# Kernel optimization log

Hardware: AMD Instinct MI355X
Metric: run time of the kernel (lower is better)

Reference implementation:

```python
import jax, jax.numpy as jnp
import numpy as np

N = 1_000_000
F_IN = 3
GRID = 480
B = 2
EPS = 1e-5


def setup_inputs() -> dict:
    key = jax.random.key(0)
    ks = jax.random.split(key, 24)
    pt_fea = jax.random.normal(ks[0], (N, F_IN), dtype=jnp.float32)
    xy_ind = jax.random.randint(ks[1], (N, 2), 0, GRID, dtype=jnp.int64)

    # batch-id prepended (F.pad(xy_ind,(1,0),value=i_batch)), then unique rows.
    batch_id = np.arange(N, dtype=np.int64) // (N // B)
    ind_np = np.asarray(xy_ind)
    lin = batch_id * (GRID * GRID) + ind_np[:, 0] * GRID + ind_np[:, 1]
    unq_lin, unq_inv = np.unique(lin, return_inverse=True)  # sorted == lexsorted rows
    unq = np.stack([unq_lin // (GRID * GRID), (unq_lin // GRID) % GRID, unq_lin % GRID], axis=1)

    def lin_w(k, fin, fout):
        return 0.05 * jax.random.normal(k, (fin, fout), dtype=jnp.float32)

    dims = [F_IN, 64, 128, 256, 128]
    params = {}
    # BN affine params: bn0 on input, bn1..bn3 after linears 1..3
    for i, d in enumerate([F_IN, 64, 128, 256]):
        params[f"bn{i}_g"] = jnp.ones((d,), jnp.float32)
        params[f"bn{i}_b"] = jnp.zeros((d,), jnp.float32)
    for i in range(4):
        params[f"W{i+1}"] = lin_w(ks[2 + i], dims[i], dims[i + 1])
        params[f"b{i+1}"] = jnp.zeros((dims[i + 1],), jnp.float32)

    return dict(pt_fea=pt_fea, xy_ind=xy_ind,
                unq=jnp.asarray(unq, jnp.int64), unq_inv=jnp.asarray(unq_inv, jnp.int32),
                **params)


def _bn(x, g, b):
    # training-mode BatchNorm1d: batch stats, biased variance
    m = jnp.mean(x, axis=0)
    v = jnp.var(x, axis=0)
    return (x - m) * jax.lax.rsqrt(v + EPS) * g + b


def reference(pt_fea, xy_ind, unq, unq_inv,
              bn0_g, bn0_b, bn1_g, bn1_b, bn2_g, bn2_b, bn3_g, bn3_b,
              W1, b1, W2, b2, W3, b3, W4, b4):
    h = _bn(pt_fea, bn0_g, bn0_b)
    h = jax.nn.relu(_bn(h @ W1 + b1, bn1_g, bn1_b))
    h = jax.nn.relu(_bn(h @ W2 + b2, bn2_g, bn2_b))
    h = jax.nn.relu(_bn(h @ W3 + b3, bn3_g, bn3_b))
    h = h @ W4 + b4  # [N, 128]
    pooled = jax.ops.segment_max(h, unq_inv, num_segments=unq.shape[0])  # [U, 128]
    return unq, pooled
```

## Files before the change

kernel.cpp:

```cpp
#include <hip/hip_runtime.h>
#include <math.h>

typedef unsigned int u32;
typedef unsigned short u16;

#define EPS 1e-5f
#define PTS 64

#define S0 0
#define Q0 16
#define S1 32
#define Q1 96
#define S2 160
#define Q2 288
#define S3 416
#define Q3 672

#define Z4S 132

typedef __attribute__((ext_vector_type(8))) short v8s;
typedef __attribute__((ext_vector_type(4))) float v4f;
typedef __attribute__((ext_vector_type(2))) unsigned int v2u;

#define MFMA(a,b,c) __builtin_amdgcn_mfma_f32_16x16x32_bf16(a,b,c,0,0,0)

#define W2H 0
#define W2L 8192
#define W3H 16384
#define W3L 49152
#define W4H 81920
#define W4L 114688
__device__ __align__(16) u16 g_wfrag[147456];

__device__ float g_acc[1024];
__device__ float g_st[1024];
__device__ int   g_is64;
__device__ int   g_inv64;
__device__ int   g_umax;
__device__ long  g_U;

__device__ __forceinline__ float bf2f(u16 b){ return __uint_as_float(((u32)b) << 16); }
__device__ __forceinline__ u16 f2bf(float f){
  u32 u = __float_as_uint(f);
  return (u16)((u + 0x7fffu + ((u >> 16) & 1u)) >> 16);
}

__device__ __forceinline__ void atomicMaxF32(float* addr, float v){
  if (v == 0.f) v = 0.f;
  if (v >= 0.f) atomicMax((int*)addr, __float_as_int(v));
  else          atomicMin((u32*)addr, __float_as_uint(v));
}

__device__ __forceinline__ void waveRedArr(float* v, int n){
  #pragma unroll
  for (int off = 32; off > 0; off >>= 1)
    for (int i = 0; i < n; ++i) v[i] += __shfl_xor(v[i], off, 64);
}

template<int FIN, int FOUT>
__device__ __forceinline__ void chunk16(const u16* hsrc, int lane,
    const float* __restrict__ W, const float* __restrict__ bias,
    int j0, float acc[16])
{
  const int j0u = __builtin_amdgcn_readfirstlane(j0);
  #pragma unroll
  for (int jj = 0; jj < 16; ++jj) acc[jj] = bias[j0u + jj];
  #pragma unroll 4
  for (int k = 0; k < FIN; ++k){
    const float hk = bf2f(hsrc[k*PTS + lane]);
    const float* Wr = W + (long)k*FOUT + j0u;
    #pragma unroll
    for (int jj = 0; jj < 16; ++jj) acc[jj] = fmaf(hk, Wr[jj], acc[jj]);
  }
}

template<int FIN, int FOUT>
__device__ __forceinline__ void chunk16_acc(const u16* hsrc, int lane,
    const float* __restrict__ W, int j0, int k0, float acc[16])
{
  const int j0u = __builtin_amdgcn_readfirstlane(j0);
  #pragma unroll 4
  for (int k = 0; k < FIN; ++k){
    const float hk = bf2f(hsrc[k*PTS + lane]);
    const float* Wr = W + (long)(k0 + k)*FOUT + j0u;
    #pragma unroll
    for (int jj = 0; jj < 16; ++jj) acc[jj] = fmaf(hk, Wr[jj], acc[jj]);
  }
}

__device__ __forceinline__ void emitStats(float acc[16], bool valid, int lane, int j0,
                                          float* bs, float* bq){
  #pragma unroll
  for (int jj = 0; jj < 16; ++jj){
    float v = valid ? acc[jj] : 0.f;
    float sq[2] = {v, v*v};
    waveRedArr(sq, 2);
    if (lane == 0){ atomicAdd(&bs[j0+jj], sq[0]); atomicAdd(&bq[j0+jj], sq[1]); }
  }
}
__device__ __forceinline__ void emitH(float acc[16], int lane, int j0u, int soff, int qoff, u16* hdst){
  #pragma unroll
  for (int jj = 0; jj < 16; ++jj){
    float z = fmaxf(acc[jj]*g_st[soff+j0u+jj] + g_st[qoff+j0u+jj], 0.f);
    hdst[(j0u+jj)*PTS + lane] = f2bf(z);
  }
}

__global__ void kreset(){
  if (threadIdx.x == 0) g_umax = 0;
  for (int i = threadIdx.x; i < 1024; i += blockDim.x) g_acc[i] = 0.f;
}

__global__ void ksniff_inv(const u32* __restrict__ w, long nwords){
  __shared__ int any;
  if (threadIdx.x == 0) any = 0;
  __syncthreads();
  for (long i = 2L*threadIdx.x + 1; i < nwords; i += 2L*blockDim.x){
    if (w[i] != 0u){ any = 1; break; }
  }
  __syncthreads();
  if (threadIdx.x == 0) g_inv64 = (any == 0) ? 1 : 0;
}

__global__ __launch_bounds__(256) void ksegU(const void* __restrict__ invv, int N){
  const int inv64 = g_inv64;
  int m = 0;
  const int stride = gridDim.x*blockDim.x;
  if (inv64){
    const long long* q = (const long long*)invv;
    for (int i = blockIdx.x*blockDim.x + threadIdx.x; i < N; i += stride)
      m = max(m, (int)q[i]);
  } else {
    const int* q = (const int*)invv;
    for (int i = blockIdx.x*blockDim.x + threadIdx.x; i < N; i += stride)
      m = max(m, q[i]);
  }
  #pragma unroll
  for (int off = 32; off > 0; off >>= 1) m = max(m, __shfl_xor(m, off, 64));
  if ((threadIdx.x & 63) == 0) atomicMax(&g_umax, m);
}

__global__ void ksniff_unq(const u32* __restrict__ w){
  __shared__ int any;
  if (threadIdx.x == 0){ g_U = (long)g_umax + 1; any = 0; }
  __syncthreads();
  const long nwords = 3L*g_U;
  for (long i = 2L*threadIdx.x + 1; i < nwords; i += 2L*blockDim.x){
    if (w[i] != 0u){ any = 1; break; }
  }
  __syncthreads();
  if (threadIdx.x == 0) g_is64 = (any == 0) ? 1 : 0;
}

__global__ void kpoolinit(float* __restrict__ out, long outSize){
  const long U = g_U;
  const long lo = 3*U;
  const long hi = (131*U < outSize) ? 131*U : outSize;
  const long i0 = (long)blockIdx.x*blockDim.x + threadIdx.x;
  const long stride = (long)gridDim.x*blockDim.x;
  for (long i = lo + i0; i < hi; i += stride) out[i] = -INFINITY;
}

__global__ void kunq(float* __restrict__ out, const void* __restrict__ unqv, long outSize){
  const long U = g_U;
  const long n = (3*U < outSize) ? 3*U : outSize;
  const long i0 = (long)blockIdx.x*blockDim.x + threadIdx.x;
  const long stride = (long)gridDim.x*blockDim.x;
  if (g_is64){
    const long long* uq = (const long long*)unqv;
    for (long i = i0; i < n; i += stride) out[i] = (float)uq[i];
  } else {
    const int* uq = (const int*)unqv;
    for (long i = i0; i < n; i += stride) out[i] = (float)uq[i];
  }
}

__global__ __launch_bounds__(256) void kstats0(const float* __restrict__ x, int N){
  __shared__ float red[4][9];
  float a[9];
  #pragma unroll
  for (int i = 0; i < 9; ++i) a[i] = 0.f;
  const int stride = gridDim.x*blockDim.x;
  for (int p = blockIdx.x*blockDim.x + threadIdx.x; p < N; p += stride){
    float v0 = x[(size_t)p*3 + 0], v1 = x[(size_t)p*3 + 1], v2 = x[(size_t)p*3 + 2];
    a[0]+=v0; a[1]+=v1; a[2]+=v2;
    a[3]+=v0*v0; a[4]+=v1*v1; a[5]+=v2*v2;
    a[6]+=v0*v1; a[7]+=v0*v2; a[8]+=v1*v2;
  }
  waveRedArr(a, 9);
  const int w = threadIdx.x >> 6, lane = threadIdx.x & 63;
  if (lane == 0){
    #pragma unroll
    for (int i = 0; i < 9; ++i) red[w][i] = a[i];
  }
  __syncthreads();
  if (threadIdx.x < 9){
    float t = 0.f;
    #pragma unroll
    for (int k = 0; k < 4; ++k) t += red[k][threadIdx.x];
    const int c = threadIdx.x;
    atomicAdd(&g_acc[(c < 3) ? (S0 + c) : (Q0 + (c - 3))], t);
  }
}

__global__ void kfin(int dim, int soff, int qoff,
                     const float* __restrict__ g, const float* __restrict__ b, float invN){
  const int j = threadIdx.x;
  if (j >= dim) return;
  const float m = g_acc[soff+j]*invN;
  const float var = fmaxf(g_acc[qoff+j]*invN - m*m, 0.f);
  const float s = g[j]*rsqrtf(var + EPS);
  g_st[soff+j] = s;
  g_st[qoff+j] = b[j] - m*s;
}

__global__ void kfin1(const float* __restrict__ g1, const float* __restrict__ b1bn,
                      const float* __restrict__ W1, const float* __restrict__ b1lin,
                      float invN){
  const int j = threadIdx.x;
  if (j >= 64) return;
  float m0[3], s0[3], t0[3];
  #pragma unroll
  for (int c = 0; c < 3; ++c){
    m0[c] = g_acc[S0+c]*invN;
    s0[c] = g_st[S0+c];
    t0[c] = g_st[Q0+c];
  }
  float C[3][3];
  C[0][0] = g_acc[Q0+0]*invN - m0[0]*m0[0];
  C[1][1] = g_acc[Q0+1]*invN - m0[1]*m0[1];
  C[2][2] = g_acc[Q0+2]*invN - m0[2]*m0[2];
  C[0][1] = C[1][0] = g_acc[Q0+3]*invN - m0[0]*m0[1];
  C[0][2] = C[2][0] = g_acc[Q0+4]*invN - m0[0]*m0[2];
  C[1][2] = C[2][1] = g_acc[Q0+5]*invN - m0[1]*m0[2];

  float wj[3] = {W1[0*64 + j], W1[1*64 + j], W1[2*64 + j]};
  float mean = b1lin[j];
  #pragma unroll
  for (int c = 0; c < 3; ++c) mean += (m0[c]*s0[c] + t0[c])*wj[c];
  float var = 0.f;
  #pragma unroll
  for (int a = 0; a < 3; ++a)
    #pragma unroll
    for (int b = 0; b < 3; ++b)
      var += wj[a]*s0[a]*wj[b]*s0[b]*C[a][b];
  var = fmaxf(var, 0.f);
  const float sc = g1[j]*rsqrtf(var + EPS);
  g_st[S1+j] = sc;
  g_st[Q1+j] = b1bn[j] - mean*sc;
}


__global__ void kprep(const float* __restrict__ W2, const float* __restrict__ W3,
                      const float* __restrict__ W4){
  int t = blockIdx.x*blockDim.x + threadIdx.x;
  int frag = t >> 6, lane = t & 63;
  if (frag >= 144) return;
  const float* W; int F, fb, kb; u16 *hi, *lo;
  if (frag < 16){
    fb = frag >> 1; kb = frag & 1; W = W2; F = 128;
    size_t o = (size_t)((fb*2 + kb)*64 + lane)*8;
    hi = g_wfrag + W2H + o; lo = g_wfrag + W2L + o;
  } else if (frag < 80){
    int f = frag - 16; fb = f >> 2; kb = f & 3; W = W3; F = 256;
    size_t o = (size_t)((fb*4 + kb)*64 + lane)*8;
    hi = g_wfrag + W3H + o; lo = g_wfrag + W3L + o;
  } else {
    int f = frag - 80; fb = f >> 3; kb = f & 7; W = W4; F = 128;
    size_t o = (size_t)((fb*8 + kb)*64 + lane)*8;
    hi = g_wfrag + W4H + o; lo = g_wfrag + W4L + o;
  }
  const int feat = fb*16 + (lane & 15);
  const int k0 = kb*32 + (lane >> 4)*8;
  #pragma unroll
  for (int jj = 0; jj < 8; ++jj){
    float wv = W[(size_t)(k0 + jj)*F + feat];
    u16 h = f2bf(wv);
    hi[jj] = h;
    lo[jj] = f2bf(wv - bf2f(h));
  }
}

__global__ __launch_bounds__(256) void kpass2m(
    const float* __restrict__ x,
    const float* __restrict__ W1, const float* __restrict__ b1,
    const float* __restrict__ b2, u16* __restrict__ z2ws, int N)
{
  __shared__ __align__(16) u16 h1f[4096];
  __shared__ __align__(16) u16 z2f[8192];
  const int tid = threadIdx.x, w = tid >> 6, lane = tid & 63;
  const int g = lane >> 4, p15 = lane & 15;

  float s2[2][4], q2[2][4];
  #pragma unroll
  for (int f = 0; f < 2; ++f)
    #pragma unroll
    for (int r = 0; r < 4; ++r){ s2[f][r] = 0.f; q2[f][r] = 0.f; }

  const int j0u = __builtin_amdgcn_readfirstlane(w*16);
  const int nb = (N + 63) >> 6;
  for (int b = blockIdx.x; b < nb; b += gridDim.x){
    const int p = b*64 + lane;
    const bool valid = p < N;
    {
      float h0[3];
      #pragma unroll
      for (int c = 0; c < 3; ++c){
        float xv = valid ? x[(size_t)p*3 + c] : 0.f;
        h0[c] = xv*g_st[S0 + c] + g_st[Q0 + c];
      }
      float acc[16];
      #pragma unroll
      for (int jj = 0; jj < 16; ++jj) acc[jj] = b1[j0u + jj];
      #pragma unroll
      for (int k = 0; k < 3; ++k){
        const float* Wr = W1 + k*64 + j0u;
        #pragma unroll
        for (int jj = 0; jj < 16; ++jj) acc[jj] = fmaf(h0[k], Wr[jj], acc[jj]);
      }
      u16 hb[16];
      #pragma unroll
      for (int jj = 0; jj < 16; ++jj)
        hb[jj] = f2bf(fmaxf(acc[jj]*g_st[S1+j0u+jj] + g_st[Q1+j0u+jj], 0.f));
      const int kb = w >> 1;
      const int lA = ((2*w) & 3)*16 + p15;
      union { v8s v; u32 u[4]; } pa, pbk;
      #pragma unroll
      for (int q = 0; q < 4; ++q){
        pa.u[q]  = (u32)hb[2*q]     | ((u32)hb[2*q+1] << 16);
        pbk.u[q] = (u32)hb[8+2*q]   | ((u32)hb[8+2*q+1] << 16);
      }
      *(v8s*)(h1f + ((kb*4 + g)*64 + lA     )*8) = pa.v;
      *(v8s*)(h1f + ((kb*4 + g)*64 + lA + 16)*8) = pbk.v;
    }
    __syncthreads();
    #pragma unroll
    for (int f = 0; f < 2; ++f){
      const int fb = w*2 + f;
      const v4f bias = *(const v4f*)(b2 + fb*16 + g*4);
      v4f acc[4];
      #pragma unroll
      for (int pb = 0; pb < 4; ++pb) acc[pb] = bias;
      #pragma unroll
      for (int kb = 0; kb < 2; ++kb){
        const v8s Ah = *(const v8s*)(g_wfrag + W2H + (size_t)((fb*2+kb)*64 + lane)*8);
        const v8s Al = *(const v8s*)(g_wfrag + W2L + (size_t)((fb*2+kb)*64 + lane)*8);
        #pragma unroll
        for (int pb = 0; pb < 4; ++pb){
          const v8s B = *(const v8s*)(h1f + ((kb*4 + pb)*64 + lane)*8);
          acc[pb] = MFMA(Ah, B, acc[pb]);
          acc[pb] = MFMA(Al, B, acc[pb]);
        }
      }
      #pragma unroll
      for (int pb = 0; pb < 4; ++pb){
        const bool pv = (b*64 + pb*16 + p15) < N;
        u16 zb[4];
        #pragma unroll
        for (int r = 0; r < 4; ++r){
          float v = pv ? acc[pb][r] : 0.f;
          s2[f][r] += v; q2[f][r] += v*v;
          zb[r] = f2bf(acc[pb][r]);
        }
        const int kb2 = fb >> 1;
        const int lp = ((2*fb + (g >> 1)) & 3)*16 + p15;
        v2u dv; dv[0] = (u32)zb[0] | ((u32)zb[1] << 16);
        dv[1] = (u32)zb[2] | ((u32)zb[3] << 16);
        *(v2u*)(z2f + ((kb2*4 + pb)*64 + lp)*8 + 4*(g & 1)) = dv;
      }
    }
    __syncthreads();
    {
      u16* dst = z2ws + (size_t)b*8192;
      #pragma unroll
      for (int i = 0; i < 4; ++i){
        const int idx = (i*256 + tid)*8;
        *(v8s*)(dst + idx) = *(const v8s*)(z2f + idx);
      }
    }
    __syncthreads();
  }
  #pragma unroll
  for (int f = 0; f < 2; ++f)
    #pragma unroll
    for (int r = 0; r < 4; ++r){
      float s = s2[f][r], q = q2[f][r];
      #pragma unroll
      for (int off = 1; off < 16; off <<= 1){
        s += __shfl_xor(s, off, 64); q += __shfl_xor(q, off, 64);
      }
      if (p15 == 0){
        const int feat = (w*2 + f)*16 + g*4 + r;
        atomicAdd(&g_acc[S2 + feat], s);
        atomicAdd(&g_acc[Q2 + feat], q);
      }
    }
}

__global__ __launch_bounds__(256) void kpass3m(
    const u16* __restrict__ z2ws, const float* __restrict__ b3,
    u16* __restrict__ z3ws, int N)
{
  __shared__ __align__(16) u16 h2f[8192];
  __shared__ __align__(16) u16 z3f[16384];
  const int tid = threadIdx.x, w = tid >> 6, lane = tid & 63;
  const int g = lane >> 4, p15 = lane & 15;

  const int k0 = w*32 + g*8;
  const v4f sA = *(const v4f*)(g_st + S2 + k0);
  const v4f sB = *(const v4f*)(g_st + S2 + k0 + 4);
  const v4f tA = *(const v4f*)(g_st + Q2 + k0);
  const v4f tB = *(const v4f*)(g_st + Q2 + k0 + 4);

  float s3[4][4], q3[4][4];
  #pragma unroll
  for (int i = 0; i < 4; ++i)
    #pragma unroll
    for (int r = 0; r < 4; ++r){ s3[i][r] = 0.f; q3[i][r] = 0.f; }

  const int nb = (N + 63) >> 6;
  for (int b = blockIdx.x; b < nb; b += gridDim.x){
    #pragma unroll
    for (int pb = 0; pb < 4; ++pb){
      union { v8s v; u32 u[4]; } in, outv;
      in.v = *(const v8s*)(z2ws + (size_t)b*8192 + ((w*4 + pb)*64 + lane)*8);
      #pragma unroll
      for (int q = 0; q < 4; ++q){
        const int e = q*2;
        float z0 = bf2f((u16)(in.u[q] & 0xFFFFu));
        float z1 = bf2f((u16)(in.u[q] >> 16));
        const float sc0 = (e   < 4) ? sA[e]   : sB[e-4];
        const float sh0 = (e   < 4) ? tA[e]   : tB[e-4];
        const float sc1 = (e+1 < 4) ? sA[e+1] : sB[e-3];
        const float sh1 = (e+1 < 4) ? tA[e+1] : tB[e-3];
        z0 = fmaxf(fmaf(z0, sc0, sh0), 0.f);
        z1 = fmaxf(fmaf(z1, sc1, sh1), 0.f);
        outv.u[q] = (u32)f2bf(z0) | ((u32)f2bf(z1) << 16);
      }
      *(v8s*)(h2f + ((w*4 + pb)*64 + lane)*8) = outv.v;
    }
    __syncthreads();
    #pragma unroll
    for (int i = 0; i < 4; ++i){
      const int fb = w*4 + i;
      const v4f bias = *(const v4f*)(b3 + fb*16 + g*4);
      v4f acc[4];
      #pragma unroll
      for (int pb = 0; pb < 4; ++pb) acc[pb] = bias;
      #pragma unroll
      for (int kb = 0; kb < 4; ++kb){
        const v8s Ah = *(const v8s*)(g_wfrag + W3H + (size_t)((fb*4+kb)*64 + lane)*8);
        const v8s Al = *(const v8s*)(g_wfrag + W3L + (size_t)((fb*4+kb)*64 + lane)*8);
        #pragma unroll
        for (int pb = 0; pb < 4; ++pb){
          const v8s B = *(const v8s*)(h2f + ((kb*4 + pb)*64 + lane)*8);
          acc[pb] = MFMA(Ah, B, acc[pb]);
          acc[pb] = MFMA(Al, B, acc[pb]);
        }
      }
      #pragma unroll
      for (int pb = 0; pb < 4; ++pb){
        const bool pv = (b*64 + pb*16 + p15) < N;
        u16 zb[4];
        #pragma unroll
        for (int r = 0; r < 4; ++r){
          float v = pv ? acc[pb][r] : 0.f;
          s3[i][r] += v; q3[i][r] += v*v;
          zb[r] = f2bf(acc[pb][r]);
        }
        const int kb3 = fb >> 1;
        const int lp = ((2*fb + (g >> 1)) & 3)*16 + p15;
        v2u dv; dv[0] = (u32)zb[0] | ((u32)zb[1] << 16);
        dv[1] = (u32)zb[2] | ((u32)zb[3] << 16);
        *(v2u*)(z3f + ((kb3*4 + pb)*64 + lp)*8 + 4*(g & 1)) = dv;
      }
    }
    __syncthreads();
    {
      u16* dst = z3ws + (size_t)b*16384;
      #pragma unroll
      for (int i2 = 0; i2 < 8; ++i2){
        const int idx = (i2*256 + tid)*8;
        *(v8s*)(dst + idx) = *(const v8s*)(z3f + idx);
      }
    }
    __syncthreads();
  }
  #pragma unroll
  for (int i = 0; i < 4; ++i)
    #pragma unroll
    for (int r = 0; r < 4; ++r){
      float s = s3[i][r], q = q3[i][r];
      #pragma unroll
      for (int off = 1; off < 16; off <<= 1){
        s += __shfl_xor(s, off, 64); q += __shfl_xor(q, off, 64);
      }
      if (p15 == 0){
        const int feat = (w*4 + i)*16 + g*4 + r;
        atomicAdd(&g_acc[S3 + feat], s);
        atomicAdd(&g_acc[Q3 + feat], q);
      }
    }
}

__global__ __launch_bounds__(256) void kpass4m(
    const void* __restrict__ unq_inv_v, const float* __restrict__ b4,
    const u16* __restrict__ z3ws, float* __restrict__ out, int N, long outSize)
{
  __shared__ __align__(16) u16 buf[16896];
  __shared__ int seg_s[64];
  u16* const h3f = buf;
  float* const z4 = (float*)buf;

  const long U = g_U;
  const int inv64 = g_inv64;
  const long loEl = 3*U;
  const long hiEl = (131*U < outSize) ? 131*U : outSize;
  const int tid = threadIdx.x, w = tid >> 6, lane = tid & 63;
  const int g = lane >> 4, p15 = lane & 15;

  const int k0a = w*64 + g*8;
  const v4f sA0 = *(const v4f*)(g_st + S3 + k0a);
  const v4f sA1 = *(const v4f*)(g_st + S3 + k0a + 4);
  const v4f tA0 = *(const v4f*)(g_st + Q3 + k0a);
  const v4f tA1 = *(const v4f*)(g_st + Q3 + k0a + 4);
  const v4f sB0 = *(const v4f*)(g_st + S3 + k0a + 32);
  const v4f sB1 = *(const v4f*)(g_st + S3 + k0a + 36);
  const v4f tB0 = *(const v4f*)(g_st + Q3 + k0a + 32);
  const v4f tB1 = *(const v4f*)(g_st + Q3 + k0a + 36);

  const int nb = (N + 63) >> 6;
  for (int b = blockIdx.x; b < nb; b += gridDim.x){
    const int p = b*64 + lane;
    const bool valid = p < N;

    #pragma unroll
    for (int kk = 0; kk < 2; ++kk){
      const int kb3 = 2*w + kk;
      #pragma unroll
      for (int pb = 0; pb < 4; ++pb){
        union { v8s v; u32 u[4]; } in, outv;
        in.v = *(const v8s*)(z3ws + (size_t)b*16384 + ((kb3*4 + pb)*64 + lane)*8);
        #pragma unroll
        for (int q = 0; q < 4; ++q){
          const int e = q*2;
          float z0 = bf2f((u16)(in.u[q] & 0xFFFFu));
          float z1 = bf2f((u16)(in.u[q] >> 16));
          const float sc0 = kk ? ((e   < 4) ? sB0[e]   : sB1[e-4]) : ((e   < 4) ? sA0[e]   : sA1[e-4]);
          const float sh0 = kk ? ((e   < 4) ? tB0[e]   : tB1[e-4]) : ((e   < 4) ? tA0[e]   : tA1[e-4]);
          const float sc1 = kk ? ((e+1 < 4) ? sB0[e+1] : sB1[e-3]) : ((e+1 < 4) ? sA0[e+1] : sA1[e-3]);
          const float sh1 = kk ? ((e+1 < 4) ? tB0[e+1] : tB1[e-3]) : ((e+1 < 4) ? tA0[e+1] : tA1[e-3]);
          z0 = fmaxf(fmaf(z0, sc0, sh0), 0.f);
          z1 = fmaxf(fmaf(z1, sc1, sh1), 0.f);
          outv.u[q] = (u32)f2bf(z0) | ((u32)f2bf(z1) << 16);
        }
        *(v8s*)(h3f + ((kb3*4 + pb)*64 + lane)*8) = outv.v;
      }
    }
    if (w == 0){
      long seg = -1;
      if (valid){
        if (inv64) seg = (long)((const long long*)unq_inv_v)[p];
        else       seg = (long)((const int*)unq_inv_v)[p];
      }
      seg_s[lane] = (seg >= 0 && seg < U &&
                     loEl + seg*128 + 128 <= hiEl) ? (int)seg : -1;
    }
    __syncthreads();

    v4f acc[2][4];
    #pragma unroll
    for (int f = 0; f < 2; ++f){
      const int fb = w*2 + f;
      const v4f bias = *(const v4f*)(b4 + fb*16 + g*4);
      #pragma unroll
      for (int pb = 0; pb < 4; ++pb) acc[f][pb] = bias;
      #pragma unroll
      for (int kb = 0; kb < 8; ++kb){
        const v8s Ah = *(const v8s*)(g_wfrag + W4H + (size_t)((fb*8+kb)*64 + lane)*8);
        const v8s Al = *(const v8s*)(g_wfrag + W4L + (size_t)((fb*8+kb)*64 + lane)*8);
        #pragma unroll
        for (int pb = 0; pb < 4; ++pb){
          const v8s B = *(const v8s*)(h3f + ((kb*4 + pb)*64 + lane)*8);
          acc[f][pb] = MFMA(Ah, B, acc[f][pb]);
          acc[f][pb] = MFMA(Al, B, acc[f][pb]);
        }
      }
    }
    __syncthreads();
    #pragma unroll
    for (int f = 0; f < 2; ++f){
      const int fb = w*2 + f;
      #pragma unroll
      for (int pb = 0; pb < 4; ++pb)
        *(v4f*)(z4 + (pb*16 + p15)*Z4S + fb*16 + g*4) = acc[f][pb];
    }
    __syncthreads();
    #pragma unroll 4
    for (int pt2 = 0; pt2 < 64; pt2 += 2){
      const int pt = pt2 + (tid >> 7);
      const int fI = tid & 127;
      const int sg = seg_s[pt];
      if (sg >= 0)
        atomicMaxF32(out + loEl + (long)sg*128 + fI, z4[pt*Z4S + fI]);
    }
    __syncthreads();
  }
}

template<int WS2>
__global__ __launch_bounds__(256) void kpass2(
    const float* __restrict__ x,
    const float* __restrict__ W1, const float* __restrict__ b1,
    const float* __restrict__ W2, const float* __restrict__ b2,
    u16* __restrict__ z2ws, int N)
{
  __shared__ u16 h1s[64*PTS];
  __shared__ float bs[256], bq[256];
  const int tid = threadIdx.x, w = tid >> 6, lane = tid & 63;
  for (int i = tid; i < 256; i += 256){ bs[i] = 0.f; bq[i] = 0.f; }
  __syncthreads();
  const int nb = (N + PTS - 1) / PTS;
  for (int b = blockIdx.x; b < nb; b += gridDim.x){
    const int p = b*PTS + lane;
    const bool valid = p < N;
    {
      float h0[3];
      #pragma unroll
      for (int c = 0; c < 3; ++c){
        float xv = valid ? x[(size_t)p*3 + c] : 0.f;
        h0[c] = xv*g_st[S0 + c] + g_st[Q0 + c];
      }
      const int j0u = __builtin_amdgcn_readfirstlane(w*16);
      float acc[16];
      #pragma unroll
      for (int jj = 0; jj < 16; ++jj) acc[jj] = b1[j0u + jj];
      #pragma unroll
      for (int k = 0; k < 3; ++k){
        const float* Wr = W1 + k*64 + j0u;
        #pragma unroll
        for (int jj = 0; jj < 16; ++jj) acc[jj] = fmaf(h0[k], Wr[jj], acc[jj]);
      }
      emitH(acc, lane, j0u, S1, Q1, h1s);
    }
    __syncthreads();
    #pragma unroll
    for (int c = 0; c < 2; ++c){
      const int j0 = w*32 + c*16;
      float acc[16];
      chunk16<64,128>(h1s, lane, W2, b2, j0, acc);
      if constexpr (WS2){
        const int j0u = __builtin_amdgcn_readfirstlane(j0);
        u16* q = z2ws + (size_t)b*8192 + (size_t)j0u*64 + lane;
        #pragma unroll
        for (int jj = 0; jj < 16; ++jj) q[jj*64] = f2bf(acc[jj]);
      }
      emitStats(acc, valid, lane, j0, bs, bq);
    }
    __syncthreads();
  }
  for (int j = tid; j < 128; j += 256){
    atomicAdd(&g_acc[S2 + j], bs[j]);
    atomicAdd(&g_acc[Q2 + j], bq[j]);
  }
}

template<int MODE>
__global__ __launch_bounds__(256) void kpass3(
    const float* __restrict__ x,
    const float* __restrict__ W1, const float* __restrict__ b1,
    const float* __restrict__ W2, const float* __restrict__ b2,
    const float* __restrict__ W3, const float* __restrict__ b3,
    u16* __restrict__ z3ws, int N)
{
  __shared__ u16 buf[12288];
  __shared__ float bs[256], bq[256];
  u16* const h2s = buf;
  u16* const h1s = buf + 8192;
  const int tid = threadIdx.x, w = tid >> 6, lane = tid & 63;
  for (int i = tid; i < 256; i += 256){ bs[i] = 0.f; bq[i] = 0.f; }
  __syncthreads();
  const int nb = (N + PTS - 1) / PTS;
  for (int b = blockIdx.x; b < nb; b += gridDim.x){
    const int p = b*PTS + lane;
    const bool valid = p < N;
    {
      float h0[3];
      #pragma unroll
      for (int c = 0; c < 3; ++c){
        float xv = valid ? x[(size_t)p*3 + c] : 0.f;
        h0[c] = xv*g_st[S0 + c] + g_st[Q0 + c];
      }
      const int j0u = __builtin_amdgcn_readfirstlane(w*16);
      float acc[16];
      #pragma unroll
      for (int jj = 0; jj < 16; ++jj) acc[jj] = b1[j0u + jj];
      #pragma unroll
      for (int k = 0; k < 3; ++k){
        const float* Wr = W1 + k*64 + j0u;
        #pragma unroll
        for (int jj = 0; jj < 16; ++jj) acc[jj] = fmaf(h0[k], Wr[jj], acc[jj]);
      }
      emitH(acc, lane, j0u, S1, Q1, h1s);
    }
    __syncthreads();
    #pragma unroll
    for (int c = 0; c < 2; ++c){
      const int j0 = w*32 + c*16;
      float acc[16];
      chunk16<64,128>(h1s, lane, W2, b2, j0, acc);
      emitH(acc, lane, __builtin_amdgcn_readfirstlane(j0), S2, Q2, h2s);
    }
    __syncthreads();
    #pragma unroll
    for (int c = 0; c < 4; ++c){
      const int j0 = w*64 + c*16;
      float acc[16];
      chunk16<128,256>(h2s, lane, W3, b3, j0, acc);
      if constexpr (MODE == 1){
        const int j0u = __builtin_amdgcn_readfirstlane(j0);
        u16* q = z3ws + (size_t)b*16384 + (size_t)j0u*64 + lane;
        #pragma unroll
        for (int jj = 0; jj < 16; ++jj) q[jj*64] = f2bf(acc[jj]);
      }
      emitStats(acc, valid, lane, j0, bs, bq);
    }
    __syncthreads();
  }
  for (int j = tid; j < 256; j += 256){
    atomicAdd(&g_acc[S3 + j], bs[j]);
    atomicAdd(&g_acc[Q3 + j], bq[j]);
  }
}

template<int MODE>
__global__ __launch_bounds__(256) void kpass4(
    const float* __restrict__ x, const void* __restrict__ unq_inv_v,
    const float* __restrict__ W1, const float* __restrict__ b1,
    const float* __restrict__ W2, const float* __restrict__ b2,
    const float* __restrict__ W3, const float* __restrict__ b3,
    const float* __restrict__ W4, const float* __restrict__ b4,
    u16* __restrict__ z3ws, float* __restrict__ out, int N, long outSize)
{
  __shared__ u16 buf[16896];
  __shared__ int seg_s[64];
  u16* const h1s = buf + 8192;
  u16* const h2s = buf;
  u16* const h3h = buf + 8192;
  u16* const h3s = buf;
  float* const z4 = (float*)buf;
  const long U = g_U;
  const int inv64 = g_inv64;
  const long loEl = 3*U;
  const long hiEl = (131*U < outSize) ? 131*U : outSize;
  const int tid = threadIdx.x, w = tid >> 6, lane = tid & 63;
  const int nb = (N + PTS - 1) / PTS;
  for (int b = blockIdx.x; b < nb; b += gridDim.x){
    const int p = b*PTS + lane;
    const bool valid = p < N;
    float accA[16], accB[16];
    if constexpr (MODE == 0){
      {
        float h0[3];
        #pragma unroll
        for (int c = 0; c < 3; ++c){
          float xv = valid ? x[(size_t)p*3 + c] : 0.f;
          h0[c] = xv*g_st[S0 + c] + g_st[Q0 + c];
        }
        const int j0u = __builtin_amdgcn_readfirstlane(w*16);
        float acc[16];
        #pragma unroll
        for (int jj = 0; jj < 16; ++jj) acc[jj] = b1[j0u + jj];
        #pragma unroll
        for (int k = 0; k < 3; ++k){
          const float* Wr = W1 + k*64 + j0u;
          #pragma unroll
          for (int jj = 0; jj < 16; ++jj) acc[jj] = fmaf(h0[k], Wr[jj], acc[jj]);
        }
        emitH(acc, lane, j0u, S1, Q1, h1s);
      }
      __syncthreads();
      #pragma unroll
      for (int c = 0; c < 2; ++c){
        const int j0 = w*32 + c*16;
        float acc[16];
        chunk16<64,128>(h1s, lane, W2, b2, j0, acc);
        emitH(acc, lane, __builtin_amdgcn_readfirstlane(j0), S2, Q2, h2s);
      }
      const int jA = __builtin_amdgcn_readfirstlane(w*32);
      #pragma unroll
      for (int jj = 0; jj < 16; ++jj){ accA[jj] = b4[jA + jj]; accB[jj] = b4[jA + 16 + jj]; }
      #pragma unroll
      for (int half = 0; half < 2; ++half){
        __syncthreads();
        #pragma unroll
        for (int c = 0; c < 2; ++c){
          const int j0 = half*128 + w*32 + c*16;
          float acc[16];
          chunk16<128,256>(h2s, lane, W3, b3, j0, acc);
          const int j0u = __builtin_amdgcn_readfirstlane(j0);
          const int r0 = j0u - half*128;
          #pragma unroll
          for (int jj = 0; jj < 16; ++jj){
            float z = fmaxf(acc[jj]*g_st[S3+j0u+jj] + g_st[Q3+j0u+jj], 0.f);
            h3h[(r0+jj)*PTS + lane] = f2bf(z);
          }
        }
        __syncthreads();
        chunk16_acc<128,128>(h3h, lane, W4, w*32,      half*128, accA);
        chunk16_acc<128,128>(h3h, lane, W4, w*32 + 16, half*128, accB);
      }
    } else {
      const int j0u = __builtin_amdgcn_readfirstlane(w*64);
      const u16* q = z3ws + (size_t)b*16384 + (size_t)j0u*64 + lane;
      #pragma unroll 8
      for (int mm = 0; mm < 64; ++mm){
        const int m = j0u + mm;
        float z = bf2f(q[mm*64]);
        z = fmaxf(z*g_st[S3 + m] + g_st[Q3 + m], 0.f);
        h3s[m*PTS + lane] = f2bf(z);
      }
      __syncthreads();
      chunk16<256,128>(h3s, lane, W4, b4, w*32,      accA);
      chunk16<256,128>(h3s, lane, W4, b4, w*32 + 16, accB);
    }
    if (w == 0){
      long seg = -1;
      if (valid){
        if (inv64) seg = (long)((const long long*)unq_inv_v)[p];
        else       seg = (long)((const int*)unq_inv_v)[p];
      }
      seg_s[lane] = (seg >= 0 && seg < U &&
                     loEl + seg*128 + 128 <= hiEl) ? (int)seg : -1;
    }
    __syncthreads();
    {
      float4* dst = (float4*)&z4[lane*Z4S + w*32];
      dst[0] = make_float4(accA[ 0],accA[ 1],accA[ 2],accA[ 3]);
      dst[1] = make_float4(accA[ 4],accA[ 5],accA[ 6],accA[ 7]);
      dst[2] = make_float4(accA[ 8],accA[ 9],accA[10],accA[11]);
      dst[3] = make_float4(accA[12],accA[13],accA[14],accA[15]);
      dst[4] = make_float4(accB[ 0],accB[ 1],accB[ 2],accB[ 3]);
      dst[5] = make_float4(accB[ 4],accB[ 5],accB[ 6],accB[ 7]);
      dst[6] = make_float4(accB[ 8],accB[ 9],accB[10],accB[11]);
      dst[7] = make_float4(accB[12],accB[13],accB[14],accB[15]);
    }
    __syncthreads();
    #pragma unroll 4
    for (int pt2 = 0; pt2 < 64; pt2 += 2){
      const int pt = pt2 + (tid >> 7);
      const int f = tid & 127;
      const int sg = seg_s[pt];
      if (sg >= 0)
        atomicMaxF32(out + loEl + (long)sg*128 + f, z4[pt*Z4S + f]);
    }
    __syncthreads();
  }
}

extern "C" void kernel_launch(void* const* d_in, const int* in_sizes, int n_in,
                              void* d_out, int out_size, void* d_ws, size_t ws_size,
                              hipStream_t stream)
{
  const float* x       = (const float*)d_in[0];
  const void*  unq     = d_in[2];
  const void*  unq_inv = d_in[3];
  const float* bn_g[4] = {(const float*)d_in[4], (const float*)d_in[6], (const float*)d_in[8], (const float*)d_in[10]};
  const float* bn_b[4] = {(const float*)d_in[5], (const float*)d_in[7], (const float*)d_in[9], (const float*)d_in[11]};
  const float* W1 = (const float*)d_in[12]; const float* b1 = (const float*)d_in[13];
  const float* W2 = (const float*)d_in[14]; const float* b2 = (const float*)d_in[15];
  const float* W3 = (const float*)d_in[16]; const float* b3 = (const float*)d_in[17];
  const float* W4 = (const float*)d_in[18]; const float* b4 = (const float*)d_in[19];

  const int N = in_sizes[0] / 3;
  float* out = (float*)d_out;
  const float invN = 1.0f / (float)N;
  const long outSize = (long)out_size;

  const size_t nb64 = (size_t)((N + 63) / 64);
  u16* z3ws = (u16*)d_ws;
  u16* z2ws = z3ws + nb64*16384;
  const size_t need1 = nb64*16384*sizeof(u16);
  const size_t need2 = nb64*(16384+8192)*sizeof(u16);
  const int wsLevel = (ws_size >= need2) ? 2 : (ws_size >= need1) ? 1 : 0;

  kreset<<<1, 1024, 0, stream>>>();
  ksniff_inv<<<1, 1024, 0, stream>>>((const u32*)unq_inv, (long)N);
  ksegU<<<512, 256, 0, stream>>>(unq_inv, N);
  ksniff_unq<<<1, 1024, 0, stream>>>((const u32*)unq);
  kpoolinit<<<2048, 256, 0, stream>>>(out, outSize);

  kstats0<<<1024, 256, 0, stream>>>(x, N);
  kfin<<<1, 256, 0, stream>>>(3, S0, Q0, bn_g[0], bn_b[0], invN);
  kfin1<<<1, 64, 0, stream>>>(bn_g[1], bn_b[1], W1, b1, invN);

  if (wsLevel == 2){
    kprep<<<36, 256, 0, stream>>>(W2, W3, W4);
    kpass2m<<<2048, 256, 0, stream>>>(x, W1, b1, b2, z2ws, N);
    kfin<<<1, 256, 0, stream>>>(128, S2, Q2, bn_g[2], bn_b[2], invN);
    kpass3m<<<1536, 256, 0, stream>>>(z2ws, b3, z3ws, N);
    kfin<<<1, 256, 0, stream>>>(256, S3, Q3, bn_g[3], bn_b[3], invN);
    kpass4m<<<1024, 256, 0, stream>>>(unq_inv, b4, z3ws, out, N, outSize);
  } else if (wsLevel == 1){
    kpass2<0><<<2048, 256, 0, stream>>>(x, W1,b1,W2,b2, z2ws, N);
    kfin<<<1, 256, 0, stream>>>(128, S2, Q2, bn_g[2], bn_b[2], invN);
    kpass3<1><<<1536, 256, 0, stream>>>(x, W1,b1,W2,b2,W3,b3, z3ws, N);
    kfin<<<1, 256, 0, stream>>>(256, S3, Q3, bn_g[3], bn_b[3], invN);
    kpass4<2><<<1024, 256, 0, stream>>>(x, unq_inv, W1,b1,W2,b2,W3,b3,W4,b4, z3ws, out, N, outSize);
  } else {
    kpass2<0><<<2048, 256, 0, stream>>>(x, W1,b1,W2,b2, z2ws, N);
    kfin<<<1, 256, 0, stream>>>(128, S2, Q2, bn_g[2], bn_b[2], invN);
    kpass3<0><<<1536, 256, 0, stream>>>(x, W1,b1,W2,b2,W3,b3, z3ws, N);
    kfin<<<1, 256, 0, stream>>>(256, S3, Q3, bn_g[3], bn_b[3], invN);
    kpass4<0><<<1024, 256, 0, stream>>>(x, unq_inv, W1,b1,W2,b2,W3,b3,W4,b4, z3ws, out, N, outSize);
  }

  kunq<<<2048, 256, 0, stream>>>(out, unq, outSize);
}
```

Baseline: 1.554 ms.

## Counting-sort points by segment so pooling reduces runs locally before writing

Adds a histogram, prefix scan and scatter that build a permutation ordering points by segment id. The MLP passes then run on the permuted order, and the final pooling pass reduces each run of equal segments within a 64-point tile in registers. Interior runs get a plain store and only runs that cross a tile boundary use an atomic max, cutting the per-element atomic traffic. The cost is four extra kernels, including a single-block serial scan over all segments, plus gathered loads of x. The old fallback paths for smaller workspace are removed.

```diff
diff --git a/kernel.cpp b/kernel.cpp
--- a/kernel.cpp
+++ b/kernel.cpp
@@ -248,6 +248,66 @@
   const float sc = g1[j]*rsqrtf(var + EPS);
   g_st[S1+j] = sc;
   g_st[Q1+j] = b1bn[j] - mean*sc;
+}
+
+__global__ void kinitsort(u32* __restrict__ cnt, u32* __restrict__ perm,
+                          int* __restrict__ segSorted, long nPos){
+  const long U = g_U;
+  const long i0 = (long)blockIdx.x*blockDim.x + threadIdx.x;
+  const long stride = (long)gridDim.x*blockDim.x;
+  for (long i = i0; i < U; i += stride) cnt[i] = 0u;
+  for (long i = i0; i < nPos; i += stride){ perm[i] = 0u; segSorted[i] = -1; }
+}
+
+__global__ __launch_bounds__(256) void khist(const void* __restrict__ invv,
+                                             u32* __restrict__ cnt, int N){
+  const int inv64 = g_inv64;
+  const long U = g_U;
+  const int stride = gridDim.x*blockDim.x;
+  for (int i = blockIdx.x*blockDim.x + threadIdx.x; i < N; i += stride){
+    long s = inv64 ? (long)((const long long*)invv)[i] : (long)((const int*)invv)[i];
+    if (s >= 0 && s < U) atomicAdd(&cnt[s], 1u);
+  }
+}
+
+__global__ __launch_bounds__(1024) void kscan(u32* __restrict__ cnt){
+  __shared__ u32 sh[1024];
+  __shared__ u32 carry;
+  const long U = g_U;
+  if (threadIdx.x == 0) carry = 0u;
+  __syncthreads();
+  for (long base = 0; base < U; base += 1024){
+    const long i = base + threadIdx.x;
+    const u32 v = (i < U) ? cnt[i] : 0u;
+    sh[threadIdx.x] = v;
+    __syncthreads();
+    #pragma unroll
+    for (int off = 1; off < 1024; off <<= 1){
+      u32 t = (threadIdx.x >= off) ? sh[threadIdx.x - off] : 0u;
+      __syncthreads();
+      sh[threadIdx.x] += t;
+      __syncthreads();
+    }
+    if (i < U) cnt[i] = carry + (sh[threadIdx.x] - v);
+    __syncthreads();
+    if (threadIdx.x == 0) carry += sh[1023];
+    __syncthreads();
+  }
+}
+
+__global__ __launch_bounds__(256) void kscatter(const void* __restrict__ invv,
+    u32* __restrict__ cnt, u32* __restrict__ perm, int* __restrict__ segSorted, int N){
+  const int inv64 = g_inv64;
+  const long U = g_U;
+  const int stride = gridDim.x*blockDim.x;
+  for (int i = blockIdx.x*blockDim.x + threadIdx.x; i < N; i += stride){
+    long s = inv64 ? (long)((const long long*)invv)[i] : (long)((const int*)invv)[i];
+    if (s >= 0 && s < U){
+      u32 pos = atomicAdd(&cnt[s], 1u);
+      perm[pos] = (u32)i;
+      segSorted[pos] = (int)s;
+    }
+  }
 }
 
 
@@ -281,10 +341,12 @@
   }
 }
 
+template<int SORT>
 __global__ __launch_bounds__(256) void kpass2m(
     const float* __restrict__ x,
     const float* __restrict__ W1, const float* __restrict__ b1,
-    const float* __restrict__ b2, u16* __restrict__ z2ws, int N)
+    const float* __restrict__ b2, u16* __restrict__ z2ws,
+    const u32* __restrict__ perm, int N)
 {
   __shared__ __align__(16) u16 h1f[4096];
   __shared__ __align__(16) u16 z2f[8192];
@@ -303,10 +365,11 @@
     const int p = b*64 + lane;
     const bool valid = p < N;
     {
+      const long ps = SORT ? (long)perm[p] : (long)p;
       float h0[3];
       #pragma unroll
       for (int c = 0; c < 3; ++c){
-        float xv = valid ? x[(size_t)p*3 + c] : 0.f;
+        float xv = valid ? x[ps*3 + c] : 0.f;
         h0[c] = xv*g_st[S0 + c] + g_st[Q0 + c];
       }
       float acc[16];
@@ -503,12 +566,15 @@
     }
 }
 
+template<int SORT>
 __global__ __launch_bounds__(256) void kpass4m(
-    const void* __restrict__ unq_inv_v, const float* __restrict__ b4,
+    const void* __restrict__ unq_inv_v, const int* __restrict__ segSorted,
+    const float* __restrict__ b4,
     const u16* __restrict__ z3ws, float* __restrict__ out, int N, long outSize)
 {
   __shared__ __align__(16) u16 buf[16896];
   __shared__ int seg_s[64];
+  __shared__ int segPrev_s, segNext_s;
   u16* const h3f = buf;
   float* const z4 = (float*)buf;
 
@@ -530,6 +596,7 @@
   const v4f tB1 = *(const v4f*)(g_st + Q3 + k0a + 36);
 
   const int nb = (N + 63) >> 6;
+  const long nPos = (long)nb*64;
   for (int b = blockIdx.x; b < nb; b += gridDim.x){
     const int p = b*64 + lane;
     const bool valid = p < N;
@@ -558,13 +625,24 @@
       }
     }
     if (w == 0){
-      long seg = -1;
-      if (valid){
-        if (inv64) seg = (long)((const long long*)unq_inv_v)[p];
-        else       seg = (long)((const int*)unq_inv_v)[p];
-      }
-      seg_s[lane] = (seg >= 0 && seg < U &&
-                     loEl + seg*128 + 128 <= hiEl) ? (int)seg : -1;
+      int sg = -1;
+      if constexpr (SORT){
+        sg = segSorted[(long)b*64 + lane];
+      } else {
+        if (valid){
+          long s = inv64 ? (long)((const long long*)unq_inv_v)[p]
+                         : (long)((const int*)unq_inv_v)[p];
+          sg = (int)s;
+        }
+      }
+      seg_s[lane] = (sg >= 0 && sg < U &&
+                     loEl + (long)sg*128 + 128 <= hiEl) ? sg : -1;
+      if constexpr (SORT){
+        if (lane == 0){
+          segPrev_s = (b > 0) ? segSorted[(long)b*64 - 1] : -2;
+          segNext_s = ((long)b*64 + 64 < nPos) ? segSorted[(long)b*64 + 64] : -2;
+        }
+      }
     }
     __syncthreads();
 
@@ -596,263 +674,33 @@
         *(v4f*)(z4 + (pb*16 + p15)*Z4S + fb*16 + g*4) = acc[f][pb];
     }
     __syncthreads();
-    #pragma unroll 4
-    for (int pt2 = 0; pt2 < 64; pt2 += 2){
-      const int pt = pt2 + (tid >> 7);
-      const int fI = tid & 127;
-      const int sg = seg_s[pt];
-      if (sg >= 0)
-        atomicMaxF32(out + loEl + (long)sg*128 + fI, z4[pt*Z4S + fI]);
-    }
-    __syncthreads();
-  }
-}
-
-template<int WS2>
-__global__ __launch_bounds__(256) void kpass2(
-    const float* __restrict__ x,
-    const float* __restrict__ W1, const float* __restrict__ b1,
-    const float* __restrict__ W2, const float* __restrict__ b2,
-    u16* __restrict__ z2ws, int N)
-{
-  __shared__ u16 h1s[64*PTS];
-  __shared__ float bs[256], bq[256];
-  const int tid = threadIdx.x, w = tid >> 6, lane = tid & 63;
-  for (int i = tid; i < 256; i += 256){ bs[i] = 0.f; bq[i] = 0.f; }
-  __syncthreads();
-  const int nb = (N + PTS - 1) / PTS;
-  for (int b = blockIdx.x; b < nb; b += gridDim.x){
-    const int p = b*PTS + lane;
-    const bool valid = p < N;
-    {
-      float h0[3];
-      #pragma unroll
-      for (int c = 0; c < 3; ++c){
-        float xv = valid ? x[(size_t)p*3 + c] : 0.f;
-        h0[c] = xv*g_st[S0 + c] + g_st[Q0 + c];
-      }
-      const int j0u = __builtin_amdgcn_readfirstlane(w*16);
-      float acc[16];
-      #pragma unroll
-      for (int jj = 0; jj < 16; ++jj) acc[jj] = b1[j0u + jj];
-      #pragma unroll
-      for (int k = 0; k < 3; ++k){
-        const float* Wr = W1 + k*64 + j0u;
-        #pragma unroll
-        for (int jj = 0; jj < 16; ++jj) acc[jj] = fmaf(h0[k], Wr[jj], acc[jj]);
-      }
-      emitH(acc, lane, j0u, S1, Q1, h1s);
-    }
-    __syncthreads();
-    #pragma unroll
-    for (int c = 0; c < 2; ++c){
-      const int j0 = w*32 + c*16;
-      float acc[16];
-      chunk16<64,128>(h1s, lane, W2, b2, j0, acc);
-      if constexpr (WS2){
-        const int j0u = __builtin_amdgcn_readfirstlane(j0);
-        u16* q = z2ws + (size_t)b*8192 + (size_t)j0u*64 + lane;
-        #pragma unroll
-        for (int jj = 0; jj < 16; ++jj) q[jj*64] = f2bf(acc[jj]);
-      }
-      emitStats(acc, valid, lane, j0, bs, bq);
-    }
-    __syncthreads();
-  }
-  for (int j = tid; j < 128; j += 256){
-    atomicAdd(&g_acc[S2 + j], bs[j]);
-    atomicAdd(&g_acc[Q2 + j], bq[j]);
-  }
-}
-
-template<int MODE>
-__global__ __launch_bounds__(256) void kpass3(
-    const float* __restrict__ x,
-    const float* __restrict__ W1, const float* __restrict__ b1,
-    const float* __restrict__ W2, const float* __restrict__ b2,
-    const float* __restrict__ W3, const float* __restrict__ b3,
-    u16* __restrict__ z3ws, int N)
-{
-  __shared__ u16 buf[12288];
-  __shared__ float bs[256], bq[256];
-  u16* const h2s = buf;
-  u16* const h1s = buf + 8192;
-  const int tid = threadIdx.x, w = tid >> 6, lane = tid & 63;
-  for (int i = tid; i < 256; i += 256){ bs[i] = 0.f; bq[i] = 0.f; }
-  __syncthreads();
-  const int nb = (N + PTS - 1) / PTS;
-  for (int b = blockIdx.x; b < nb; b += gridDim.x){
-    const int p = b*PTS + lane;
-    const bool valid = p < N;
-    {
-      float h0[3];
-      #pragma unroll
-      for (int c = 0; c < 3; ++c){
-        float xv = valid ? x[(size_t)p*3 + c] : 0.f;
-        h0[c] = xv*g_st[S0 + c] + g_st[Q0 + c];
-      }
-      const int j0u = __builtin_amdgcn_readfirstlane(w*16);
-      float acc[16];
-      #pragma unroll
-      for (int jj = 0; jj < 16; ++jj) acc[jj] = b1[j0u + jj];
-      #pragma unroll
-      for (int k = 0; k < 3; ++k){
-        const float* Wr = W1 + k*64 + j0u;
-        #pragma unroll
-        for (int jj = 0; jj < 16; ++jj) acc[jj] = fmaf(h0[k], Wr[jj], acc[jj]);
-      }
-      emitH(acc, lane, j0u, S1, Q1, h1s);
-    }
-    __syncthreads();
-    #pragma unroll
-    for (int c = 0; c < 2; ++c){
-      const int j0 = w*32 + c*16;
-      float acc[16];
-      chunk16<64,128>(h1s, lane, W2, b2, j0, acc);
-      emitH(acc, lane, __builtin_amdgcn_readfirstlane(j0), S2, Q2, h2s);
-    }
-    __syncthreads();
-    #pragma unroll
-    for (int c = 0; c < 4; ++c){
-      const int j0 = w*64 + c*16;
-      float acc[16];
-      chunk16<128,256>(h2s, lane, W3, b3, j0, acc);
-      if constexpr (MODE == 1){
-        const int j0u = __builtin_amdgcn_readfirstlane(j0);
-        u16* q = z3ws + (size_t)b*16384 + (size_t)j0u*64 + lane;
-        #pragma unroll
-        for (int jj = 0; jj < 16; ++jj) q[jj*64] = f2bf(acc[jj]);
-      }
-      emitStats(acc, valid, lane, j0, bs, bq);
-    }
-    __syncthreads();
-  }
-  for (int j = tid; j < 256; j += 256){
-    atomicAdd(&g_acc[S3 + j], bs[j]);
-    atomicAdd(&g_acc[Q3 + j], bq[j]);
-  }
-}
-
-template<int MODE>
-__global__ __launch_bounds__(256) void kpass4(
-    const float* __restrict__ x, const void* __restrict__ unq_inv_v,
-    const float* __restrict__ W1, const float* __restrict__ b1,
-    const float* __restrict__ W2, const float* __restrict__ b2,
-    const float* __restrict__ W3, const float* __restrict__ b3,
-    const float* __restrict__ W4, const float* __restrict__ b4,
-    u16* __restrict__ z3ws, float* __restrict__ out, int N, long outSize)
-{
-  __shared__ u16 buf[16896];
-  __shared__ int seg_s[64];
-  u16* const h1s = buf + 8192;
-  u16* const h2s = buf;
-  u16* const h3h = buf + 8192;
-  u16* const h3s = buf;
-  float* const z4 = (float*)buf;
-  const long U = g_U;
-  const int inv64 = g_inv64;
-  const long loEl = 3*U;
-  const long hiEl = (131*U < outSize) ? 131*U : outSize;
-  const int tid = threadIdx.x, w = tid >> 6, lane = tid & 63;
-  const int nb = (N + PTS - 1) / PTS;
-  for (int b = blockIdx.x; b < nb; b += gridDim.x){
-    const int p = b*PTS + lane;
-    const bool valid = p < N;
-    float accA[16], accB[16];
-    if constexpr (MODE == 0){
-      {
-        float h0[3];
-        #pragma unroll
-        for (int c = 0; c < 3; ++c){
-          float xv = valid ? x[(size_t)p*3 + c] : 0.f;
-          h0[c] = xv*g_st[S0 + c] + g_st[Q0 + c];
-        }
-        const int j0u = __builtin_amdgcn_readfirstlane(w*16);
-        float acc[16];
-        #pragma unroll
-        for (int jj = 0; jj < 16; ++jj) acc[jj] = b1[j0u + jj];
-        #pragma unroll
-        for (int k = 0; k < 3; ++k){
-          const float* Wr = W1 + k*64 + j0u;
-          #pragma unroll
-          for (int jj = 0; jj < 16; ++jj) acc[jj] = fmaf(h0[k], Wr[jj], acc[jj]);
-        }
-        emitH(acc, lane, j0u, S1, Q1, h1s);
-      }
-      __syncthreads();
-      #pragma unroll
-      for (int c = 0; c < 2; ++c){
-        const int j0 = w*32 + c*16;
-        float acc[16];
-        chunk16<64,128>(h1s, lane, W2, b2, j0, acc);
-        emitH(acc, lane, __builtin_amdgcn_readfirstlane(j0), S2, Q2, h2s);
-      }
-      const int jA = __builtin_amdgcn_readfirstlane(w*32);
-      #pragma unroll
-      for (int jj = 0; jj < 16; ++jj){ accA[jj] = b4[jA + jj]; accB[jj] = b4[jA + 16 + jj]; }
-      #pragma unroll
-      for (int half = 0; half < 2; ++half){
-        __syncthreads();
-        #pragma unroll
-        for (int c = 0; c < 2; ++c){
-          const int j0 = half*128 + w*32 + c*16;
-          float acc[16];
-          chunk16<128,256>(h2s, lane, W3, b3, j0, acc);
-          const int j0u = __builtin_amdgcn_readfirstlane(j0);
-          const int r0 = j0u - half*128;
-          #pragma unroll
-          for (int jj = 0; jj < 16; ++jj){
-            float z = fmaxf(acc[jj]*g_st[S3+j0u+jj] + g_st[Q3+j0u+jj], 0.f);
-            h3h[(r0+jj)*PTS + lane] = f2bf(z);
-          }
-        }
-        __syncthreads();
-        chunk16_acc<128,128>(h3h, lane, W4, w*32,      half*128, accA);
-        chunk16_acc<128,128>(h3h, lane, W4, w*32 + 16, half*128, accB);
+
+    if constexpr (SORT){
+      const int sPrev = segPrev_s, sNext = segNext_s;
+      #pragma unroll 1
+      for (int pt2 = 0; pt2 < 64; pt2 += 2){
+        const int pt = pt2 + (tid >> 7);
+        const int fI = tid & 127;
+        const int sg = seg_s[pt];
+        if (sg >= 0 && (pt == 0 || seg_s[pt-1] != sg)){
+          float m = z4[pt*Z4S + fI];
+          int e = pt + 1;
+          while (e < 64 && seg_s[e] == sg){ m = fmaxf(m, z4[e*Z4S + fI]); ++e; }
+          const long row = loEl + (long)sg*128 + fI;
+          const bool bnd = (pt == 0 && sPrev == sg) || (e == 64 && sNext == sg);
+          if (bnd) atomicMaxF32(out + row, m);
+          else     out[row] = (m == 0.f) ? 0.f : m;
+        }
       }
     } else {
-      const int j0u = __builtin_amdgcn_readfirstlane(w*64);
-      const u16* q = z3ws + (size_t)b*16384 + (size_t)j0u*64 + lane;
-      #pragma unroll 8
-      for (int mm = 0; mm < 64; ++mm){
-        const int m = j0u + mm;
-        float z = bf2f(q[mm*64]);
-        z = fmaxf(z*g_st[S3 + m] + g_st[Q3 + m], 0.f);
-        h3s[m*PTS + lane] = f2bf(z);
-      }
-      __syncthreads();
-      chunk16<256,128>(h3s, lane, W4, b4, w*32,      accA);
-      chunk16<256,128>(h3s, lane, W4, b4, w*32 + 16, accB);
-    }
-    if (w == 0){
-      long seg = -1;
-      if (valid){
-        if (inv64) seg = (long)((const long long*)unq_inv_v)[p];
-        else       seg = (long)((const int*)unq_inv_v)[p];
-      }
-      seg_s[lane] = (seg >= 0 && seg < U &&
-                     loEl + seg*128 + 128 <= hiEl) ? (int)seg : -1;
-    }
-    __syncthreads();
-    {
-      float4* dst = (float4*)&z4[lane*Z4S + w*32];
-      dst[0] = make_float4(accA[ 0],accA[ 1],accA[ 2],accA[ 3]);
-      dst[1] = make_float4(accA[ 4],accA[ 5],accA[ 6],accA[ 7]);
-      dst[2] = make_float4(accA[ 8],accA[ 9],accA[10],accA[11]);
-      dst[3] = make_float4(accA[12],accA[13],accA[14],accA[15]);
-      dst[4] = make_float4(accB[ 0],accB[ 1],accB[ 2],accB[ 3]);
-      dst[5] = make_float4(accB[ 4],accB[ 5],accB[ 6],accB[ 7]);
-      dst[6] = make_float4(accB[ 8],accB[ 9],accB[10],accB[11]);
-      dst[7] = make_float4(accB[12],accB[13],accB[14],accB[15]);
-    }
-    __syncthreads();
-    #pragma unroll 4
-    for (int pt2 = 0; pt2 < 64; pt2 += 2){
-      const int pt = pt2 + (tid >> 7);
-      const int f = tid & 127;
-      const int sg = seg_s[pt];
-      if (sg >= 0)
-        atomicMaxF32(out + loEl + (long)sg*128 + f, z4[pt*Z4S + f]);
+      #pragma unroll 4
+      for (int pt2 = 0; pt2 < 64; pt2 += 2){
+        const int pt = pt2 + (tid >> 7);
+        const int fI = tid & 127;
+        const int sg = seg_s[pt];
+        if (sg >= 0)
+          atomicMaxF32(out + loEl + (long)sg*128 + fI, z4[pt*Z4S + fI]);
+      }
     }
     __syncthreads();
   }
@@ -878,11 +726,15 @@
   const long outSize = (long)out_size;
 
   const size_t nb64 = (size_t)((N + 63) / 64);
+  const size_t nPos = nb64 * 64;
   u16* z3ws = (u16*)d_ws;
   u16* z2ws = z3ws + nb64*16384;
-  const size_t need1 = nb64*16384*sizeof(u16);
+  u32* permW = (u32*)(z2ws + nb64*8192);
+  int* segSortedW = (int*)(permW + nPos);
+  u32* cntW = (u32*)(segSortedW + nPos);
   const size_t need2 = nb64*(16384+8192)*sizeof(u16);
-  const int wsLevel = (ws_size >= need2) ? 2 : (ws_size >= need1) ? 1 : 0;
+  const size_t need3 = need2 + (nPos*2 + (size_t)N)*4;
+  const int wsLevel = (ws_size >= need3) ? 3 : (ws_size >= need2) ? 2 : 0;
 
   kreset<<<1, 1024, 0, stream>>>();
   ksniff_inv<<<1, 1024, 0, stream>>>((const u32*)unq_inv, (long)N);
@@ -894,25 +746,24 @@
   kfin<<<1, 256, 0, stream>>>(3, S0, Q0, bn_g[0], bn_b[0], invN);
   kfin1<<<1, 64, 0, stream>>>(bn_g[1], bn_b[1], W1, b1, invN);
 
-  if (wsLevel == 2){
+  if (wsLevel == 3){
+    kinitsort<<<2048, 256, 0, stream>>>(cntW, permW, segSortedW, (long)nPos);
+    khist<<<1024, 256, 0, stream>>>(unq_inv, cntW, N);
+    kscan<<<1, 1024, 0, stream>>>(cntW);
+    kscatter<<<1024, 256, 0, stream>>>(unq_inv, cntW, permW, segSortedW, N);
     kprep<<<36, 256, 0, stream>>>(W2, W3, W4);
-    kpass2m<<<2048, 256, 0, stream>>>(x, W1, b1, b2, z2ws, N);
+    kpass2m<1><<<2048, 256, 0, stream>>>(x, W1, b1, b2, z2ws, permW, N);
     kfin<<<1, 256, 0, stream>>>(128, S2, Q2, bn_g[2], bn_b[2], invN);
     kpass3m<<<1536, 256, 0, stream>>>(z2ws, b3, z3ws, N);
     kfin<<<1, 256, 0, stream>>>(256, S3, Q3, bn_g[3], bn_b[3], invN);
-    kpass4m<<<1024, 256, 0, stream>>>(unq_inv, b4, z3ws, out, N, outSize);
-  } else if (wsLevel == 1){
-    kpass2<0><<<2048, 256, 0, stream>>>(x, W1,b1,W2,b2, z2ws, N);
+    kpass4m<1><<<1024, 256, 0, stream>>>(unq_inv, segSortedW, b4, z3ws, out, N, outSize);
+  } else {
+    kprep<<<36, 256, 0, stream>>>(W2, W3, W4);
+    kpass2m<0><<<2048, 256, 0, stream>>>(x, W1, b1, b2, z2ws, permW, N);
     kfin<<<1, 256, 0, stream>>>(128, S2, Q2, bn_g[2], bn_b[2], invN);
-    kpass3<1><<<1536, 256, 0, stream>>>(x, W1,b1,W2,b2,W3,b3, z3ws, N);
+    kpass3m<<<1536, 256, 0, stream>>>(z2ws, b3, z3ws, N);
     kfin<<<1, 256, 0, stream>>>(256, S3, Q3, bn_g[3], bn_b[3], invN);
-    kpass4<2><<<1024, 256, 0, stream>>>(x, unq_inv, W1,b1,W2,b2,W3,b3,W4,b4, z3ws, out, N, outSize);
-  } else {
-    kpass2<0><<<2048, 256, 0, stream>>>(x, W1,b1,W2,b2, z2ws, N);
-    kfin<<<1, 256, 0, stream>>>(128, S2, Q2, bn_g[2], bn_b[2], invN);
-    kpass3<0><<<1536, 256, 0, stream>>>(x, W1,b1,W2,b2,W3,b3, z3ws, N);
-    kfin<<<1, 256, 0, stream>>>(256, S3, Q3, bn_g[3], bn_b[3], invN);
-    kpass4<0><<<1024, 256, 0, stream>>>(x, unq_inv, W1,b1,W2,b2,W3,b3,W4,b4, z3ws, out, N, outSize);
+    kpass4m<0><<<1024, 256, 0, stream>>>(unq_inv, segSortedW, b4, z3ws, out, N, outSize);
   }
 
   kunq<<<2048, 256, 0, stream>>>(out, unq, outSize);
```

Result: slower. 2.714 ms (+74.7%).
